# Kernel optimization log

Measured on AMD Instinct MI355X. Metric: run time of the kernel, lower is better.

The kernel has to match this reference:

```python
import jax, jax.numpy as jnp
import numpy as np

N_ITER = 3  # affine-invariant Karcher mean iterations (mean_options['n_iterations'])
EPS = 1e-12


def _sym(A):
    return 0.5 * (A + jnp.swapaxes(A, -1, -2))


def _eig_fun(A, fn):
    # Apply spectral function fn to symmetric matrix/matrices A: V diag(fn(w)) V^T
    w, V = jnp.linalg.eigh(A)
    return jnp.einsum('...ij,...j,...kj->...ik', V, fn(w), V)


def _logm(A):
    return _eig_fun(A, lambda w: jnp.log(jnp.maximum(w, EPS)))


def _expm(A):
    return _eig_fun(A, jnp.exp)


def _sqrtm(A):
    return _eig_fun(A, lambda w: jnp.sqrt(jnp.maximum(w, 0.0)))


def _invsqrtm(A):
    return _eig_fun(A, lambda w: 1.0 / jnp.sqrt(jnp.maximum(w, EPS)))


def _affine_invariant_mean(data, n_iterations):
    # Karcher mean: init at arithmetic mean, fixed-point iterations on the manifold
    M = jnp.mean(data, axis=0)
    for _ in range(n_iterations):
        Ms = _sqrtm(M)
        Mi = _invsqrtm(M)
        T = jnp.mean(_logm(Mi @ data @ Mi), axis=0)  # (n, n) tangent mean
        M = Ms @ _expm(T) @ Ms
    return _sym(M)


def setup_inputs() -> dict:
    key = jax.random.key(0)
    k1, k2 = jax.random.split(key)
    B, n = 8192, 64
    X = jax.random.normal(k1, (B, n, n), dtype=jnp.float32)
    # SPD batch: X X^T / n + 0.1 I
    data = jnp.einsum('bij,bkj->bik', X, X) / n + 0.1 * jnp.eye(n, dtype=jnp.float32)
    bias_param = 0.1 * jax.random.normal(k2, (n, n), dtype=jnp.float32)
    return {"data": data, "bias_param": bias_param}


def reference(data, bias_param):
    # 1) batch mean on the SPD manifold (affine-invariant Karcher mean)
    mean = _affine_invariant_mean(data, N_ITER)
    # 2) whitening: G data G with G = mean^{-1/2}
    G = _invsqrtm(mean)
    data_normalized = G @ data @ G
    # 3) bias congruence: Covbias = expm(sym(bias_param)) (log-Euclidean param),
    #    S = Covbias^{1/2} = expm(sym(bias_param)/2); out = S X S
    S = _eig_fun(_sym(bias_param), lambda w: jnp.exp(0.5 * w))
    return S @ data_normalized @ S
```

## Files before the change

### kernel.cpp

```cpp
#include <hip/hip_runtime.h>
#include <cmath>

#ifndef M_PI
#define M_PI 3.14159265358979323846
#endif

#define K_CHEB 48
#define A_CHEB 0.05
#define B_CHEB 14.0
#define PS_S 7
#define PS_Q 6

typedef __attribute__((ext_vector_type(8))) short bhalf8;
typedef __attribute__((ext_vector_type(16))) float f32x16;

struct PSArg {
  float mid, invhalf;
  float a[PS_Q + 1][PS_S];
};


__device__ __forceinline__ unsigned cvt_pk_bf16(float a, float b) {
  unsigned r;
  asm("v_cvt_pk_bf16_f32 %0, %1, %2" : "=v"(r) : "v"(a), "v"(b));
  return r;
}

__device__ __forceinline__ void split4_store(short* __restrict__ Xh, short* __restrict__ Xl,
                                             int off, float v0, float v1, float v2, float v3) {
  unsigned h01 = cvt_pk_bf16(v0, v1);
  unsigned h23 = cvt_pk_bf16(v2, v3);
  float r0 = v0 - __uint_as_float(h01 << 16);
  float r1 = v1 - __uint_as_float(h01 & 0xffff0000u);
  float r2 = v2 - __uint_as_float(h23 << 16);
  float r3 = v3 - __uint_as_float(h23 & 0xffff0000u);
  unsigned l01 = cvt_pk_bf16(r0, r1);
  unsigned l23 = cvt_pk_bf16(r2, r3);
  *(uint2*)(Xh + off) = make_uint2(h01, h23);
  *(uint2*)(Xl + off) = make_uint2(l01, l23);
}


__device__ __forceinline__ void stage64(const float* __restrict__ g, float* __restrict__ s, int tid) {
#pragma unroll
  for (int r = 0; r < 4; r++) {
    int idx = tid + 256 * r;
    *(float4*)(s + 4 * idx) = *(const float4*)(g + 4 * idx);
  }
}

__device__ __forceinline__ void store_tile(float* __restrict__ S, int r0, int c0, const float t[16]) {
#pragma unroll
  for (int i = 0; i < 4; i++)
    *(float4*)(S + (r0 + i) * 64 + c0) = *(const float4*)(&t[4 * i]);
}

__device__ __forceinline__ void gemm_tile_sym(const float* __restrict__ A, const float* __restrict__ B,
                                              int r0, int c0, float t[16]) {
#pragma unroll
  for (int i = 0; i < 16; i++) t[i] = 0.f;
#pragma unroll 4
  for (int k = 0; k < 64; k += 4) {
    float a[16], b[16];
#pragma unroll
    for (int kk = 0; kk < 4; kk++) {
      *(float4*)(&a[4 * kk]) = *(const float4*)(A + (k + kk) * 64 + r0);
      *(float4*)(&b[4 * kk]) = *(const float4*)(B + (k + kk) * 64 + c0);
    }
#pragma unroll
    for (int kk = 0; kk < 4; kk++)
#pragma unroll
      for (int i = 0; i < 4; i++)
#pragma unroll
        for (int j = 0; j < 4; j++)
          t[4 * i + j] += a[4 * kk + i] * b[4 * kk + j];
  }
}

__device__ __forceinline__ float trace_bcast(const float* __restrict__ s) {
  const int l = threadIdx.x & 63;
  float d = s[l * 65];
#pragma unroll
  for (int o = 32; o > 0; o >>= 1) d += __shfl_down(d, o, 64);
  return __shfl(d, 0, 64) * (1.f / 64.f);
}


__global__ __launch_bounds__(256) void reduce_mean8(const float* __restrict__ data,
                                                    float* __restrict__ part) {
  const size_t base = (size_t)blockIdx.x * 8 * 4096;
  const int tid = threadIdx.x;
#pragma unroll
  for (int r = 0; r < 4; r++) {
    int idx = tid + 256 * r;
    float4 s = make_float4(0.f, 0.f, 0.f, 0.f);
#pragma unroll
    for (int m = 0; m < 8; m++) {
      float4 v = *(const float4*)(data + base + (size_t)m * 4096 + 4 * idx);
      s.x += v.x; s.y += v.y; s.z += v.z; s.w += v.w;
    }
    *(float4*)(part + (size_t)blockIdx.x * 4096 + 4 * idx) = s;
  }
}

__global__ __launch_bounds__(256) void reduce_cols(const float* __restrict__ part,
                                                   float* __restrict__ outv,
                                                   int nparts, float scale) {
  __shared__ float s[3][64];
  const int jj = threadIdx.x & 63, gg = threadIdx.x >> 6;
  const int j = (blockIdx.x << 6) + jj;
  float sum = 0.f;
  for (int g = gg; g < nparts; g += 4)
    sum += part[(size_t)g * 4096 + j];
  if (gg) s[gg - 1][jj] = sum;
  __syncthreads();
  if (gg == 0) outv[j] = (sum + s[0][jj] + s[1][jj] + s[2][jj]) * scale;
}


#define MAT 4096

__device__ __forceinline__ void load_afrags(const short* __restrict__ Xh, const short* __restrict__ Xl,
                                            const int ao[4], bhalf8 ah[4], bhalf8 al[4]) {
#pragma unroll
  for (int kb = 0; kb < 4; kb++) {
    ah[kb] = *(const bhalf8*)(Xh + ao[kb]);
    al[kb] = *(const bhalf8*)(Xl + ao[kb]);
  }
}

__device__ __forceinline__ f32x16 prod3(const bhalf8 ah[4], const bhalf8 al[4],
                                        const short* __restrict__ Bh, const short* __restrict__ Bl,
                                        const int bo[4]) {
  f32x16 a0, a1;
#pragma unroll
  for (int t = 0; t < 16; t++) { a0[t] = 0.f; a1[t] = 0.f; }
#pragma unroll
  for (int kb = 0; kb < 4; kb++) {
    bhalf8 bh = *(const bhalf8*)(Bh + bo[kb]);
    bhalf8 bl = *(const bhalf8*)(Bl + bo[kb]);
    if (kb & 1) {
      a1 = __builtin_amdgcn_mfma_f32_32x32x16_bf16(ah[kb], bh, a1, 0, 0, 0);
      a1 = __builtin_amdgcn_mfma_f32_32x32x16_bf16(ah[kb], bl, a1, 0, 0, 0);
      a1 = __builtin_amdgcn_mfma_f32_32x32x16_bf16(al[kb], bh, a1, 0, 0, 0);
    } else {
      a0 = __builtin_amdgcn_mfma_f32_32x32x16_bf16(ah[kb], bh, a0, 0, 0, 0);
      a0 = __builtin_amdgcn_mfma_f32_32x32x16_bf16(ah[kb], bl, a0, 0, 0, 0);
      a0 = __builtin_amdgcn_mfma_f32_32x32x16_bf16(al[kb], bh, a0, 0, 0, 0);
    }
  }
  return a0 + a1;
}

__device__ __forceinline__ void tstore16(short* __restrict__ Xh, short* __restrict__ Xl,
                                         int bcol, int xb7, int R, int half, const f32x16 v) {
#pragma unroll
  for (int g = 0; g < 4; g++) {
    int off = bcol * 64 + 8 * ((4 * R + g) ^ xb7) + 4 * half;
    split4_store(Xh, Xl, off, v[4 * g + 0], v[4 * g + 1], v[4 * g + 2], v[4 * g + 3]);
  }
}

__device__ __forceinline__ void stage_split(const float* __restrict__ g64,
                                            short* __restrict__ Xh, short* __restrict__ Xl,
                                            int tid) {
#pragma unroll
  for (int i = 0; i < 4; i++) {
    int idx = tid + 256 * i;
    float4 v = *(const float4*)(g64 + 4 * idx);
    int row = idx >> 4, c4 = idx & 15;
    int off = row * 64 + 8 * ((c4 >> 1) ^ (row & 7)) + 4 * (c4 & 1);
    split4_store(Xh, Xl, off, v.x, v.y, v.z, v.w);
  }
}

__global__ __launch_bounds__(256, 2) void cheb_ps(const float* __restrict__ data,
                                                  const float* __restrict__ Mi,
                                                  float* __restrict__ partial,
                                                  PSArg co) {
  extern __shared__ __align__(16) short smem[];
  short* sMh  = smem;
  short* sMl  = sMh + MAT;
  short* sAh  = sMl + MAT;
  short* sAl  = sAh + MAT;
  short* sB0h = sAl + MAT;
  short* sB0l = sB0h + MAT;
  short* sB1h = sB0l + MAT;
  short* sB1l = sB1h + MAT;

  const int tid = threadIdx.x;
  const int lane = tid & 63, wv = tid >> 6;
  const int R = wv >> 1, C = wv & 1;
  const int ln31 = lane & 31, half = lane >> 5;
  const int arow = 32 * R + ln31;
  const int bcol = 32 * C + ln31;
  int ao[4], bo[4];
#pragma unroll
  for (int kb = 0; kb < 4; kb++) {
    ao[kb] = arow * 64 + 8 * ((half + 2 * kb) ^ (arow & 7));
    bo[kb] = bcol * 64 + 8 * ((half + 2 * kb) ^ (bcol & 7));
  }
  const int xb7 = bcol & 7;
  const int dsel = bcol - 32 * R - 4 * half;

  stage_split(Mi, sMh, sMl, tid);

  f32x16 accTm;
#pragma unroll
  for (int t = 0; t < 16; t++) accTm[t] = 0.f;

  bhalf8 ah[4], al[4];
  __syncthreads();

#pragma unroll 1
  for (int m = 0; m < 8; m++) {
    stage_split(data + ((size_t)blockIdx.x * 8 + m) * 4096, sAh, sAl, tid);
    __syncthreads();

    load_afrags(sAh, sAl, ao, ah, al);
    f32x16 acc = prod3(ah, al, sMh, sMl, bo);
    tstore16(sB0h, sB0l, bcol, xb7, R, half, acc);
    __syncthreads();

    load_afrags(sMh, sMl, ao, ah, al);
    acc = prod3(ah, al, sB0h, sB0l, bo);
    f32x16 T1;
#pragma unroll
    for (int g = 0; g < 4; g++)
#pragma unroll
      for (int t = 0; t < 4; t++) {
        float a = acc[4 * g + t];
        if (8 * g + t == dsel) a -= co.mid;
        T1[4 * g + t] = a * co.invhalf;
      }
    tstore16(sAh, sAl, bcol, xb7, R, half, T1);
    __syncthreads();

    load_afrags(sAh, sAl, ao, ah, al);

    f32x16 T2, T3, T4, T5, T6;
    acc = prod3(ah, al, sAh, sAl, bo);
#pragma unroll
    for (int g = 0; g < 4; g++)
#pragma unroll
      for (int t = 0; t < 4; t++)
        T2[4 * g + t] = 2.f * acc[4 * g + t] - ((8 * g + t == dsel) ? 1.f : 0.f);
    tstore16(sB0h, sB0l, bcol, xb7, R, half, T2);
    __syncthreads();

    acc = prod3(ah, al, sB0h, sB0l, bo);
#pragma unroll
    for (int t = 0; t < 16; t++) T3[t] = 2.f * acc[t] - T1[t];
    tstore16(sB1h, sB1l, bcol, xb7, R, half, T3);
    __syncthreads();

    acc = prod3(ah, al, sB1h, sB1l, bo);
#pragma unroll
    for (int t = 0; t < 16; t++) T4[t] = 2.f * acc[t] - T2[t];
    tstore16(sB0h, sB0l, bcol, xb7, R, half, T4);
    __syncthreads();

    acc = prod3(ah, al, sB0h, sB0l, bo);
#pragma unroll
    for (int t = 0; t < 16; t++) T5[t] = 2.f * acc[t] - T3[t];
    tstore16(sB1h, sB1l, bcol, xb7, R, half, T5);
    __syncthreads();

    acc = prod3(ah, al, sB1h, sB1l, bo);
#pragma unroll
    for (int t = 0; t < 16; t++) T6[t] = 2.f * acc[t] - T4[t];
    tstore16(sB0h, sB0l, bcol, xb7, R, half, T6);
    __syncthreads();

    acc = prod3(ah, al, sB0h, sB0l, bo);
    f32x16 Y7;
#pragma unroll
    for (int t = 0; t < 16; t++) Y7[t] = 2.f * acc[t] - T5[t];
    tstore16(sAh, sAl, bcol, xb7, R, half, Y7);
    __syncthreads();

    load_afrags(sAh, sAl, ao, ah, al);
    f32x16 bq1, bq2;
#pragma unroll
    for (int g = 0; g < 4; g++)
#pragma unroll
      for (int t = 0; t < 4; t++) {
        int i = 4 * g + t;
        float v = co.a[6][1] * T1[i] + co.a[6][2] * T2[i] + co.a[6][3] * T3[i]
                + co.a[6][4] * T4[i] + co.a[6][5] * T5[i] + co.a[6][6] * T6[i];
        if (8 * g + t == dsel) v += co.a[6][0];
        bq1[i] = v; bq2[i] = 0.f;
      }
    tstore16(sB1h, sB1l, bcol, xb7, R, half, bq1);
    __syncthreads();

#pragma unroll
    for (int q = 5; q >= 1; q--) {
      const short* rh = (q & 1) ? sB1h : sB0h;
      const short* rl = (q & 1) ? sB1l : sB0l;
      short* wh = (q & 1) ? sB0h : sB1h;
      short* wl = (q & 1) ? sB0l : sB1l;
      acc = prod3(ah, al, rh, rl, bo);
      f32x16 nb;
#pragma unroll
      for (int g = 0; g < 4; g++)
#pragma unroll
        for (int t = 0; t < 4; t++) {
          int i = 4 * g + t;
          float gq = co.a[q][1] * T1[i] + co.a[q][2] * T2[i] + co.a[q][3] * T3[i]
                   + co.a[q][4] * T4[i] + co.a[q][5] * T5[i] + co.a[q][6] * T6[i];
          if (8 * g + t == dsel) gq += co.a[q][0];
          nb[i] = gq + 2.f * acc[i] - bq2[i];
        }
      bq2 = bq1; bq1 = nb;
      tstore16(wh, wl, bcol, xb7, R, half, bq1);
      __syncthreads();
    }

    acc = prod3(ah, al, sB0h, sB0l, bo);
#pragma unroll
    for (int g = 0; g < 4; g++)
#pragma unroll
      for (int t = 0; t < 4; t++) {
        int i = 4 * g + t;
        float g0 = co.a[0][1] * T1[i] + co.a[0][2] * T2[i] + co.a[0][3] * T3[i]
                 + co.a[0][4] * T4[i] + co.a[0][5] * T5[i] + co.a[0][6] * T6[i];
        if (8 * g + t == dsel) g0 += co.a[0][0];
        accTm[i] += g0 + acc[i] - bq2[i];
      }
    __syncthreads();
  }

  float* pp = partial + (size_t)blockIdx.x * 4096;
#pragma unroll
  for (int g = 0; g < 4; g++)
#pragma unroll
    for (int t = 0; t < 4; t++)
      pp[(32 * R + 8 * g + 4 * half + t) * 64 + bcol] = accTm[4 * g + t];
}


__global__ __launch_bounds__(256) void invsqrt_series(const float* __restrict__ Min,
                                                      float* __restrict__ MiOut,
                                                      float* __restrict__ MsOut) {
  __shared__ float sM[4096], sE[4096], sE2[4096], sE3[4096];
  const int tid = threadIdx.x;
  const int r0 = (tid >> 4) << 2, c0 = (tid & 15) << 2;

  stage64(Min, sM, tid);
  __syncthreads();
  const float csh = trace_bcast(sM);
  const float invc = 1.f / csh;
  for (int idx = tid; idx < 4096; idx += 256) {
    int r = idx >> 6, c = idx & 63;
    sE[idx] = 0.5f * (sM[idx] + sM[c * 64 + r]) * invc - ((r == c) ? 1.f : 0.f);
  }
  __syncthreads();

  float t[16];
  gemm_tile_sym(sE, sE, r0, c0, t);  store_tile(sE2, r0, c0, t); __syncthreads();
  gemm_tile_sym(sE2, sE, r0, c0, t); store_tile(sE3, r0, c0, t); __syncthreads();
  gemm_tile_sym(sE2, sE2, r0, c0, t); store_tile(sM, r0, c0, t); __syncthreads();
  float t5[16];
  gemm_tile_sym(sE2, sE3, r0, c0, t5);

  const float sc = sqrtf(csh), rsc = 1.f / sc;
#pragma unroll
  for (int i = 0; i < 4; i++)
#pragma unroll
    for (int j = 0; j < 4; j++) {
      int off = (r0 + i) * 64 + (c0 + j);
      float d = ((r0 + i) == (c0 + j)) ? 1.f : 0.f;
      float e = sE[off], e2 = sE2[off], e3 = sE3[off], e4 = sM[off], e5 = t5[4 * i + j];
      float mi = (d - 0.5f * e + 0.375f * e2 - 0.3125f * e3 + 0.2734375f * e4 - 0.24609375f * e5) * rsc;
      float ms = (d + 0.5f * e - 0.125f * e2 + 0.0625f * e3 - 0.0390625f * e4 + 0.02734375f * e5) * sc;
      MiOut[off] = mi;
      MsOut[off] = ms;
    }
}


__device__ void taylor_expm8(const float* __restrict__ sA, float* __restrict__ sR,
                             int tid, int r0, int c0, float postscale) {
  for (int idx = tid; idx < 4096; idx += 256) {
    int r = idx >> 6, c = idx & 63;
    sR[idx] = ((r == c) ? 1.f : 0.f) + sA[idx] * 0.125f;
  }
  __syncthreads();
  float t[16];
#pragma unroll 1
  for (int k = 7; k >= 1; k--) {
    gemm_tile_sym(sA, sR, r0, c0, t);
    __syncthreads();
    const float inv = 1.f / (float)k;
    const float fin = (k == 1) ? postscale : 1.f;
#pragma unroll
    for (int i = 0; i < 4; i++)
#pragma unroll
      for (int j = 0; j < 4; j++) {
        int off = (r0 + i) * 64 + (c0 + j);
        float d = ((r0 + i) == (c0 + j)) ? 1.f : 0.f;
        sR[off] = (d + t[4 * i + j] * inv) * fin;
      }
    __syncthreads();
  }
}


__global__ __launch_bounds__(256) void expm_invsqrt(const float* __restrict__ Tin,
                                                    const float* __restrict__ Msin,
                                                    float* __restrict__ MiOut,
                                                    float* __restrict__ MsOut) {
  __shared__ float s0[4096], s1[4096], s2[4096], s3[4096], s4[4096];
  const int tid = threadIdx.x;
  const int r0 = (tid >> 4) << 2, c0 = (tid & 15) << 2;
  float t[16];

  stage64(Tin, s0, tid);
  __syncthreads();
  const float mu = trace_bcast(s0);
  for (int idx = tid; idx < 4096; idx += 256) {
    int r = idx >> 6, c = idx & 63;
    s1[idx] = 0.5f * (s0[idx] + s0[c * 64 + r]) - ((r == c) ? mu : 0.f);
  }
  __syncthreads();
  taylor_expm8(s1, s2, tid, r0, c0, expf(mu));

  stage64(Msin, s0, tid);
  __syncthreads();
  gemm_tile_sym(s2, s0, r0, c0, t);
  store_tile(s3, r0, c0, t);
  __syncthreads();
  gemm_tile_sym(s0, s3, r0, c0, t);
  store_tile(s4, r0, c0, t);
  __syncthreads();

  const float csh = trace_bcast(s4);
  const float invc = 1.f / csh;
  for (int idx = tid; idx < 4096; idx += 256) {
    int r = idx >> 6, c = idx & 63;
    s0[idx] = 0.5f * (s4[idx] + s4[c * 64 + r]) * invc - ((r == c) ? 1.f : 0.f);
  }
  __syncthreads();
  gemm_tile_sym(s0, s0, r0, c0, t);  store_tile(s1, r0, c0, t); __syncthreads();
  gemm_tile_sym(s1, s0, r0, c0, t);  store_tile(s2, r0, c0, t); __syncthreads();
  gemm_tile_sym(s1, s1, r0, c0, t);  store_tile(s3, r0, c0, t); __syncthreads();
  float t5[16];
  gemm_tile_sym(s1, s2, r0, c0, t5);

  const float sc = sqrtf(csh), rsc = 1.f / sc;
#pragma unroll
  for (int i = 0; i < 4; i++)
#pragma unroll
    for (int j = 0; j < 4; j++) {
      int off = (r0 + i) * 64 + (c0 + j);
      float d = ((r0 + i) == (c0 + j)) ? 1.f : 0.f;
      float e = s0[off], e2 = s1[off], e3 = s2[off], e4 = s3[off], e5 = t5[4 * i + j];
      float mi = (d - 0.5f * e + 0.375f * e2 - 0.3125f * e3 + 0.2734375f * e4 - 0.24609375f * e5) * rsc;
      float ms = (d + 0.5f * e - 0.125f * e2 + 0.0625f * e3 - 0.0390625f * e4 + 0.02734375f * e5) * sc;
      MiOut[off] = mi;
      MsOut[off] = ms;
    }
}

__global__ __launch_bounds__(256) void bias_expm_P(const float* __restrict__ bias,
                                                   const float* __restrict__ Gin,
                                                   float* __restrict__ Pout) {
  __shared__ float sA[4096], sR[4096], sB[4096];
  const int tid = threadIdx.x;
  const int r0 = (tid >> 4) << 2, c0 = (tid & 15) << 2;

  stage64(bias, sB, tid);
  __syncthreads();
  for (int idx = tid; idx < 4096; idx += 256) {
    int r = idx >> 6, c = idx & 63;
    sA[idx] = 0.0625f * (sB[idx] + sB[c * 64 + r]);
  }
  __syncthreads();
  taylor_expm8(sA, sR, tid, r0, c0, 1.f);

  float t[16];
  gemm_tile_sym(sR, sR, r0, c0, t);
  store_tile(sB, r0, c0, t);
  __syncthreads();
  gemm_tile_sym(sB, sB, r0, c0, t);
  store_tile(sR, r0, c0, t);
  stage64(Gin, sA, tid);
  __syncthreads();
  gemm_tile_sym(sR, sA, r0, c0, t);
#pragma unroll
  for (int i = 0; i < 4; i++)
    *(float4*)(Pout + (r0 + i) * 64 + c0) = *(const float4*)(&t[4 * i]);
}

__global__ __launch_bounds__(256) void final_out(const float* __restrict__ data,
                                                 const float* __restrict__ Pin,
                                                 float* __restrict__ out) {
  __shared__ float sPT[4096], sD[4096], sT[4096];
  const int tid = threadIdx.x;
  const int r0 = (tid >> 4) << 2, c0 = (tid & 15) << 2;

  for (int idx = tid; idx < 4096; idx += 256) {
    int r = idx >> 6, c = idx & 63;
    sPT[c * 64 + r] = Pin[idx];
  }
  __syncthreads();
  float t[16];
#pragma unroll 1
  for (int m = 0; m < 8; m++) {
    size_t b = (size_t)blockIdx.x * 8 + m;
    stage64(data + b * 4096, sD, tid);
    __syncthreads();
    gemm_tile_sym(sD, sPT, r0, c0, t);
    store_tile(sT, r0, c0, t);
    __syncthreads();
    gemm_tile_sym(sPT, sT, r0, c0, t);
    float* ob = out + b * 4096;
#pragma unroll
    for (int i = 0; i < 4; i++)
      *(float4*)(ob + (r0 + i) * 64 + c0) = *(const float4*)(&t[4 * i]);
    __syncthreads();
  }
}


extern "C" void kernel_launch(void* const* d_in, const int* in_sizes, int n_in,
                              void* d_out, int out_size, void* d_ws, size_t ws_size,
                              hipStream_t stream) {
  const float* data = (const float*)d_in[0];
  const float* bias = (const float*)d_in[1];
  float* out = (float*)d_out;

  float* part = out;
  float* M  = (float*)d_ws;
  float* Mi = M + 4096;
  float* Ms = Mi + 4096;
  float* Tm = Ms + 4096;
  float* P  = Tm + 4096;

  static bool attr_done = false;
  if (!attr_done) {
    hipFuncSetAttribute(reinterpret_cast<const void*>(cheb_ps),
                        hipFuncAttributeMaxDynamicSharedMemorySize,
                        8 * MAT * (int)sizeof(short));
    attr_done = true;
  }
  const int lds_bytes = 8 * MAT * (int)sizeof(short);

  PSArg co;
  {
    const double a = A_CHEB, b = B_CHEB;
    const int N = 256;
    double c[64] = {0};
    for (int j = 0; j <= K_CHEB; j++) {
      double s = 0.0;
      for (int k = 0; k < N; k++) {
        double th = M_PI * (k + 0.5) / N;
        double x = 0.5 * (a + b) + 0.5 * (b - a) * std::cos(th);
        s += std::log(x) * std::cos(j * th);
      }
      c[j] = 2.0 * s / N;
    }
    c[0] *= 0.5;
    double aa[PS_Q + 1][PS_S] = {};
    for (int q = PS_Q; q >= 1; --q) {
      for (int r = PS_S - 1; r >= 1; --r) {
        int k = q * PS_S + r;
        double av = 2.0 * c[k];
        aa[q][r] = av;
        c[k] -= av * 0.5;
        c[q * PS_S - r] -= av * 0.5;
      }
      aa[q][0] = c[q * PS_S];
      c[q * PS_S] = 0.0;
    }
    for (int r = 0; r < PS_S; r++) aa[0][r] = c[r];
    co.mid = (float)(0.5 * (a + b));
    co.invhalf = (float)(2.0 / (b - a));
    for (int q = 0; q <= PS_Q; q++)
      for (int r = 0; r < PS_S; r++) co.a[q][r] = (float)aa[q][r];
  }

  reduce_mean8<<<1024, 256, 0, stream>>>(data, part);
  reduce_cols<<<64, 256, 0, stream>>>(part, M, 1024, 1.f / 8192.f);
  invsqrt_series<<<1, 256, 0, stream>>>(M, Mi, Ms);

  for (int it = 0; it < 3; ++it) {
    cheb_ps<<<1024, 256, lds_bytes, stream>>>(data, Mi, part, co);
    reduce_cols<<<64, 256, 0, stream>>>(part, Tm, 1024, 1.f / 8192.f);
    expm_invsqrt<<<1, 256, 0, stream>>>(Tm, Ms, Mi, Ms);
  }

  bias_expm_P<<<1, 256, 0, stream>>>(bias, Mi, P);
  final_out<<<1024, 256, 0, stream>>>(data, P, out);
}
```

Baseline: 1.441 ms.

## Use Chebyshev doubling identities, padded LDS layout, and fewer barriers in cheb_ps

Rewrites the Chebyshev basis build so T3–T6 and Y7 come from products with T2 (T_{m+n} = 2 T_m T_n − T_{|m−n|}). This allows two independent matrix products per barrier phase and removes several __syncthreads. It also replaces the XOR-swizzled LDS layout with a padded row stride of 72 and drops the split dual-accumulator MFMA chain. Mi is now re-staged from global memory on every matrix iteration to free a buffer, and LDS use per block grows because of the padding. The doubling identities may change rounding behaviour slightly.

```diff
diff --git a/kernel.cpp b/kernel.cpp
--- a/kernel.cpp
+++ b/kernel.cpp
@@ -118,45 +118,40 @@
 }
 
 
-#define MAT 4096
+#define LDX 72
+#define MAT (64 * LDX)
 
 __device__ __forceinline__ void load_afrags(const short* __restrict__ Xh, const short* __restrict__ Xl,
-                                            const int ao[4], bhalf8 ah[4], bhalf8 al[4]) {
+                                            int aoff, bhalf8 ah[4], bhalf8 al[4]) {
 #pragma unroll
   for (int kb = 0; kb < 4; kb++) {
-    ah[kb] = *(const bhalf8*)(Xh + ao[kb]);
-    al[kb] = *(const bhalf8*)(Xl + ao[kb]);
+    ah[kb] = *(const bhalf8*)(Xh + aoff + 16 * kb);
+    al[kb] = *(const bhalf8*)(Xl + aoff + 16 * kb);
   }
 }
 
 __device__ __forceinline__ f32x16 prod3(const bhalf8 ah[4], const bhalf8 al[4],
                                         const short* __restrict__ Bh, const short* __restrict__ Bl,
-                                        const int bo[4]) {
-  f32x16 a0, a1;
-#pragma unroll
-  for (int t = 0; t < 16; t++) { a0[t] = 0.f; a1[t] = 0.f; }
+                                        int boff) {
+  f32x16 acc;
+#pragma unroll
+  for (int t = 0; t < 16; t++) acc[t] = 0.f;
 #pragma unroll
   for (int kb = 0; kb < 4; kb++) {
-    bhalf8 bh = *(const bhalf8*)(Bh + bo[kb]);
-    bhalf8 bl = *(const bhalf8*)(Bl + bo[kb]);
-    if (kb & 1) {
-      a1 = __builtin_amdgcn_mfma_f32_32x32x16_bf16(ah[kb], bh, a1, 0, 0, 0);
-      a1 = __builtin_amdgcn_mfma_f32_32x32x16_bf16(ah[kb], bl, a1, 0, 0, 0);
-      a1 = __builtin_amdgcn_mfma_f32_32x32x16_bf16(al[kb], bh, a1, 0, 0, 0);
-    } else {
-      a0 = __builtin_amdgcn_mfma_f32_32x32x16_bf16(ah[kb], bh, a0, 0, 0, 0);
-      a0 = __builtin_amdgcn_mfma_f32_32x32x16_bf16(ah[kb], bl, a0, 0, 0, 0);
-      a0 = __builtin_amdgcn_mfma_f32_32x32x16_bf16(al[kb], bh, a0, 0, 0, 0);
-    }
-  }
-  return a0 + a1;
+    bhalf8 bh = *(const bhalf8*)(Bh + boff + 16 * kb);
+    bhalf8 bl = *(const bhalf8*)(Bl + boff + 16 * kb);
+    acc = __builtin_amdgcn_mfma_f32_32x32x16_bf16(ah[kb], bh, acc, 0, 0, 0);
+    acc = __builtin_amdgcn_mfma_f32_32x32x16_bf16(ah[kb], bl, acc, 0, 0, 0);
+    acc = __builtin_amdgcn_mfma_f32_32x32x16_bf16(al[kb], bh, acc, 0, 0, 0);
+  }
+  return acc;
 }
 
 __device__ __forceinline__ void tstore16(short* __restrict__ Xh, short* __restrict__ Xl,
-                                         int bcol, int xb7, int R, int half, const f32x16 v) {
+                                         int bcol, int R, int half, const f32x16 v) {
 #pragma unroll
   for (int g = 0; g < 4; g++) {
-    int off = bcol * 64 + 8 * ((4 * R + g) ^ xb7) + 4 * half;
+    int off = bcol * LDX + 32 * R + 8 * g + 4 * half;
     split4_store(Xh, Xl, off, v[4 * g + 0], v[4 * g + 1], v[4 * g + 2], v[4 * g + 3]);
   }
 }
@@ -168,9 +163,8 @@
   for (int i = 0; i < 4; i++) {
     int idx = tid + 256 * i;
     float4 v = *(const float4*)(g64 + 4 * idx);
-    int row = idx >> 4, c4 = idx & 15;
-    int off = row * 64 + 8 * ((c4 >> 1) ^ (row & 7)) + 4 * (c4 & 1);
-    split4_store(Xh, Xl, off, v.x, v.y, v.z, v.w);
+    int row = idx >> 4, col = (idx & 15) << 2;
+    split4_store(Xh, Xl, row * LDX + col, v.x, v.y, v.z, v.w);
   }
 }
 
@@ -179,51 +173,39 @@
                                                   float* __restrict__ partial,
                                                   PSArg co) {
   extern __shared__ __align__(16) short smem[];
-  short* sMh  = smem;
-  short* sMl  = sMh + MAT;
-  short* sAh  = sMl + MAT;
-  short* sAl  = sAh + MAT;
-  short* sB0h = sAl + MAT;
-  short* sB0l = sB0h + MAT;
-  short* sB1h = sB0l + MAT;
-  short* sB1l = sB1h + MAT;
+  short* s0h = smem;            short* s0l = s0h + MAT;
+  short* s1h = s0l + MAT;       short* s1l = s1h + MAT;
+  short* s2h = s1l + MAT;       short* s2l = s2h + MAT;
+  short* s3h = s2l + MAT;       short* s3l = s3h + MAT;
 
   const int tid = threadIdx.x;
   const int lane = tid & 63, wv = tid >> 6;
   const int R = wv >> 1, C = wv & 1;
   const int ln31 = lane & 31, half = lane >> 5;
-  const int arow = 32 * R + ln31;
+  const int aoff = (32 * R + ln31) * LDX + half * 8;
   const int bcol = 32 * C + ln31;
-  int ao[4], bo[4];
-#pragma unroll
-  for (int kb = 0; kb < 4; kb++) {
-    ao[kb] = arow * 64 + 8 * ((half + 2 * kb) ^ (arow & 7));
-    bo[kb] = bcol * 64 + 8 * ((half + 2 * kb) ^ (bcol & 7));
-  }
-  const int xb7 = bcol & 7;
+  const int boff = bcol * LDX + half * 8;
   const int dsel = bcol - 32 * R - 4 * half;
 
-  stage_split(Mi, sMh, sMl, tid);
-
   f32x16 accTm;
 #pragma unroll
   for (int t = 0; t < 16; t++) accTm[t] = 0.f;
 
   bhalf8 ah[4], al[4];
-  __syncthreads();
 
 #pragma unroll 1
   for (int m = 0; m < 8; m++) {
-    stage_split(data + ((size_t)blockIdx.x * 8 + m) * 4096, sAh, sAl, tid);
-    __syncthreads();
-
-    load_afrags(sAh, sAl, ao, ah, al);
-    f32x16 acc = prod3(ah, al, sMh, sMl, bo);
-    tstore16(sB0h, sB0l, bcol, xb7, R, half, acc);
-    __syncthreads();
-
-    load_afrags(sMh, sMl, ao, ah, al);
-    acc = prod3(ah, al, sB0h, sB0l, bo);
+    stage_split(data + ((size_t)blockIdx.x * 8 + m) * 4096, s0h, s0l, tid);
+    stage_split(Mi, s1h, s1l, tid);
+    __syncthreads();
+
+    load_afrags(s0h, s0l, aoff, ah, al);
+    f32x16 acc = prod3(ah, al, s1h, s1l, boff);
+    tstore16(s2h, s2l, bcol, R, half, acc);
+    __syncthreads();
+
+    load_afrags(s1h, s1l, aoff, ah, al);
+    acc = prod3(ah, al, s2h, s2l, boff);
     f32x16 T1;
 #pragma unroll
     for (int g = 0; g < 4; g++)
@@ -233,53 +215,50 @@
         if (8 * g + t == dsel) a -= co.mid;
         T1[4 * g + t] = a * co.invhalf;
       }
-    tstore16(sAh, sAl, bcol, xb7, R, half, T1);
-    __syncthreads();
-
-    load_afrags(sAh, sAl, ao, ah, al);
-
-    f32x16 T2, T3, T4, T5, T6;
-    acc = prod3(ah, al, sAh, sAl, bo);
+    tstore16(s3h, s3l, bcol, R, half, T1);
+    __syncthreads();
+
+    load_afrags(s3h, s3l, aoff, ah, al);
+    acc = prod3(ah, al, s3h, s3l, boff);
+    f32x16 T2;
 #pragma unroll
     for (int g = 0; g < 4; g++)
 #pragma unroll
       for (int t = 0; t < 4; t++)
         T2[4 * g + t] = 2.f * acc[4 * g + t] - ((8 * g + t == dsel) ? 1.f : 0.f);
-    tstore16(sB0h, sB0l, bcol, xb7, R, half, T2);
-    __syncthreads();
-
-    acc = prod3(ah, al, sB0h, sB0l, bo);
+    tstore16(s0h, s0l, bcol, R, half, T2);
+    __syncthreads();
+
+    load_afrags(s0h, s0l, aoff, ah, al);
+    acc          = prod3(ah, al, s3h, s3l, boff);
+    f32x16 acc2  = prod3(ah, al, s0h, s0l, boff);
+    f32x16 T3, T4;
 #pragma unroll
     for (int t = 0; t < 16; t++) T3[t] = 2.f * acc[t] - T1[t];
-    tstore16(sB1h, sB1l, bcol, xb7, R, half, T3);
-    __syncthreads();
-
-    acc = prod3(ah, al, sB1h, sB1l, bo);
-#pragma unroll
-    for (int t = 0; t < 16; t++) T4[t] = 2.f * acc[t] - T2[t];
-    tstore16(sB0h, sB0l, bcol, xb7, R, half, T4);
-    __syncthreads();
-
-    acc = prod3(ah, al, sB0h, sB0l, bo);
-#pragma unroll
-    for (int t = 0; t < 16; t++) T5[t] = 2.f * acc[t] - T3[t];
-    tstore16(sB1h, sB1l, bcol, xb7, R, half, T5);
-    __syncthreads();
-
-    acc = prod3(ah, al, sB1h, sB1l, bo);
-#pragma unroll
-    for (int t = 0; t < 16; t++) T6[t] = 2.f * acc[t] - T4[t];
-    tstore16(sB0h, sB0l, bcol, xb7, R, half, T6);
-    __syncthreads();
-
-    acc = prod3(ah, al, sB0h, sB0l, bo);
+#pragma unroll
+    for (int g = 0; g < 4; g++)
+#pragma unroll
+      for (int t = 0; t < 4; t++)
+        T4[4 * g + t] = 2.f * acc2[4 * g + t] - ((8 * g + t == dsel) ? 1.f : 0.f);
+    tstore16(s2h, s2l, bcol, R, half, T3);
+    tstore16(s1h, s1l, bcol, R, half, T4);
+    __syncthreads();
+
+    acc  = prod3(ah, al, s2h, s2l, boff);
+    acc2 = prod3(ah, al, s1h, s1l, boff);
+    f32x16 T5, T6;
+#pragma unroll
+    for (int t = 0; t < 16; t++) T5[t] = 2.f * acc[t] - T1[t];
+#pragma unroll
+    for (int t = 0; t < 16; t++) T6[t] = 2.f * acc2[t] - T2[t];
+    tstore16(s3h, s3l, bcol, R, half, T5);
+    __syncthreads();
+
+    acc = prod3(ah, al, s3h, s3l, boff);
     f32x16 Y7;
 #pragma unroll
-    for (int t = 0; t < 16; t++) Y7[t] = 2.f * acc[t] - T5[t];
-    tstore16(sAh, sAl, bcol, xb7, R, half, Y7);
-    __syncthreads();
-
-    load_afrags(sAh, sAl, ao, ah, al);
+    for (int t = 0; t < 16; t++) Y7[t] = 2.f * acc[t] - T3[t];
+    tstore16(s1h, s1l, bcol, R, half, Y7);
     f32x16 bq1, bq2;
 #pragma unroll
     for (int g = 0; g < 4; g++)
@@ -291,16 +270,17 @@
         if (8 * g + t == dsel) v += co.a[6][0];
         bq1[i] = v; bq2[i] = 0.f;
       }
-    tstore16(sB1h, sB1l, bcol, xb7, R, half, bq1);
-    __syncthreads();
-
+    tstore16(s0h, s0l, bcol, R, half, bq1);
+    __syncthreads();
+
+    load_afrags(s1h, s1l, aoff, ah, al);
 #pragma unroll
     for (int q = 5; q >= 1; q--) {
-      const short* rh = (q & 1) ? sB1h : sB0h;
-      const short* rl = (q & 1) ? sB1l : sB0l;
-      short* wh = (q & 1) ? sB0h : sB1h;
-      short* wl = (q & 1) ? sB0l : sB1l;
-      acc = prod3(ah, al, rh, rl, bo);
+      const short* rh = (q & 1) ? s0h : s2h;
+      const short* rl = (q & 1) ? s0l : s2l;
+      short* wh = (q & 1) ? s2h : s0h;
+      short* wl = (q & 1) ? s2l : s0l;
+      acc = prod3(ah, al, rh, rl, boff);
       f32x16 nb;
 #pragma unroll
       for (int g = 0; g < 4; g++)
@@ -313,11 +293,11 @@
           nb[i] = gq + 2.f * acc[i] - bq2[i];
         }
       bq2 = bq1; bq1 = nb;
-      tstore16(wh, wl, bcol, xb7, R, half, bq1);
+      tstore16(wh, wl, bcol, R, half, bq1);
       __syncthreads();
     }
 
-    acc = prod3(ah, al, sB0h, sB0l, bo);
+    acc = prod3(ah, al, s2h, s2l, boff);
 #pragma unroll
     for (int g = 0; g < 4; g++)
 #pragma unroll
@@ -328,7 +308,6 @@
         if (8 * g + t == dsel) g0 += co.a[0][0];
         accTm[i] += g0 + acc[i] - bq2[i];
       }
-    __syncthreads();
   }
 
   float* pp = partial + (size_t)blockIdx.x * 4096;
```

Result: faster. 1.405 ms (-2.5%).
